# Kernel tuning notes

Measured on AMD Instinct MI355X. Metric: run time of the kernel, lower is better.

## Reference

```python
import jax, jax.numpy as jnp
import numpy as np

B, LQ, S, D, H = 8, 1024, 256, 1024, 16
HD = D // H
LN_EPS = 1e-5


def layer_norm(x, g, b):
    m = jnp.mean(x, axis=-1, keepdims=True)
    v = jnp.mean((x - m) ** 2, axis=-1, keepdims=True)
    return (x - m) / jnp.sqrt(v + LN_EPS) * g + b


def setup_inputs() -> dict:
    key = jax.random.key(0)
    ks = jax.random.split(key, 12)
    sc = 0.02
    p = lambda k, shp: jax.random.normal(k, shp, dtype=jnp.float32) * sc
    return {
        "memory": jax.random.normal(ks[0], (B, LQ, D // 2), dtype=jnp.float32),
        "gaze_features": jax.random.normal(ks[1], (B, LQ, D // 2), dtype=jnp.float32),
        "text_features": jax.random.normal(ks[2], (B, S, D), dtype=jnp.float32),
        "w_in": p(ks[3], (3 * D, D)),  # packed q,k,v in_proj (torch MHA layout)
        "b_in": jnp.zeros((3 * D,), jnp.float32),
        "w_o": p(ks[4], (D, D)),
        "b_o": jnp.zeros((D,), jnp.float32),
        "w1": p(ks[5], (D, D)),
        "b1": jnp.zeros((D,), jnp.float32),
        "w2": p(ks[6], (D, D)),
        "b2": jnp.zeros((D,), jnp.float32),
        "g1": jnp.ones((D,), jnp.float32),
        "be1": jnp.zeros((D,), jnp.float32),
        "g2": jnp.ones((D,), jnp.float32),
        "be2": jnp.zeros((D,), jnp.float32),
    }


def reference(memory, gaze_features, text_features, w_in, b_in, w_o, b_o,
              w1, b1, w2, b2, g1, be1, g2, be2):
    combined = jnp.concatenate([memory, gaze_features], axis=-1)  # [B, LQ, D]
    wq, wk, wv = w_in[:D], w_in[D:2 * D], w_in[2 * D:]
    bq, bk, bv = b_in[:D], b_in[D:2 * D], b_in[2 * D:]

    q = (combined @ wq.T + bq).reshape(B, LQ, H, HD)
    k = (text_features @ wk.T + bk).reshape(B, S, H, HD)
    v = (text_features @ wv.T + bv).reshape(B, S, H, HD)

    scores = jnp.einsum("bqhd,bkhd->bhqk", q, k) / jnp.sqrt(jnp.float32(HD))
    attn_w = jax.nn.softmax(scores, axis=-1)
    ctx = jnp.einsum("bhqk,bkhd->bqhd", attn_w, v).reshape(B, LQ, D)
    attn_output = ctx @ w_o.T + b_o  # [B, LQ, D]

    # dual FFN branches share linear1/linear2 (as in the source); dropout = eval identity
    ffn = jax.nn.relu(attn_output @ w1.T + b1) @ w2.T + b2
    refpoint_embed = layer_norm(ffn, g1, be1)
    tgt = layer_norm(ffn, g2, be2)

    # vectorized box decode (replaces the per-element Python loop)
    s = jax.nn.sigmoid(attn_output[..., :4])
    xc, yc, w, h = s[..., 0], s[..., 1], s[..., 2], s[..., 3]
    init_box_proposal = jnp.stack(
        [xc - w / 2, yc - h / 2, xc + w / 2, yc + h / 2], axis=-1)  # [B, LQ, 4]

    return refpoint_embed, tgt, init_box_proposal
```

## Files before the change

kernel.cpp:

```cpp
#include <hip/hip_runtime.h>


typedef unsigned short u16;
typedef unsigned int u32;
typedef __bf16 bf16x8 __attribute__((ext_vector_type(8)));
typedef float f32x4 __attribute__((ext_vector_type(4)));
typedef u16 u16x4 __attribute__((ext_vector_type(4)));

struct CvtArgs { const void* in[15]; };

__device__ __forceinline__ u16 f2bf(float f) {
  u32 u = __builtin_bit_cast(u32, f);
  u += 0x7fffu + ((u >> 16) & 1u);
  return (u16)(u >> 16);
}
__device__ __forceinline__ float bf2f(u16 h) {
  u32 u = ((u32)h) << 16;
  return __builtin_bit_cast(float, u);
}

struct WsPtrs {
  u16 *c_mem, *c_gaze, *c_text, *c_win, *c_bin, *c_wo, *c_bo, *c_w1, *c_b1,
      *c_w2, *c_b2, *c_g1, *c_be1, *c_g2, *c_be2;
  u16 *q, *k, *v, *ctx, *woT, *wf, *bfb, *h1, *ffnb;
};
__device__ __forceinline__ WsPtrs wsp(u16* C) {
  WsPtrs w;
  w.c_mem = C;                 w.c_gaze = C + 4194304;   w.c_text = C + 8388608;
  w.c_win = C + 10485760;      w.c_bin = C + 13631488;   w.c_wo = C + 13634560;
  w.c_bo = C + 14683136;       w.c_w1 = C + 14684160;    w.c_b1 = C + 15732736;
  w.c_w2 = C + 15733760;       w.c_b2 = C + 16782336;    w.c_g1 = C + 16783360;
  w.c_be1 = C + 16784384;      w.c_g2 = C + 16785408;    w.c_be2 = C + 16786432;
  u16* B2 = C + 16787488;
  w.q = B2;                    w.k = B2 + 8388608;       w.v = B2 + 10485760;
  w.ctx = B2 + 12582912;
  w.woT = B2 + 20971520;
  w.wf  = B2 + 22020096;
  w.bfb = B2 + 23068672;
  w.h1  = B2 + 29360128;
  w.ffnb = B2;
  return w;
}

__device__ __forceinline__ void cvt_chunk(bool f32in, u16* dst,
                                          const void* const* srcs, u32 c8) {
  const u32 cum[16] = {0u, 4194304u, 8388608u, 10485760u, 13631488u, 13634560u,
                       14683136u, 14684160u, 15732736u, 15733760u, 16782336u,
                       16783360u, 16784384u, 16785408u, 16786432u, 16787456u};
  u32 base = c8 * 8u;
  int idx = 0;
#pragma unroll
  for (int i = 1; i < 15; ++i) if (base >= cum[i]) idx = i;
  u32 off = base - cum[idx];
  if (f32in) {
    const float* s = (const float*)srcs[idx] + off;
    float4 a = ((const float4*)s)[0];
    float4 b = ((const float4*)s)[1];
    u16 t[8] = {f2bf(a.x), f2bf(a.y), f2bf(a.z), f2bf(a.w),
                f2bf(b.x), f2bf(b.y), f2bf(b.z), f2bf(b.w)};
    *(uint4*)(dst + base) = *(const uint4*)t;
  } else {
    *(uint4*)(dst + base) = *(const uint4*)((const u16*)srcs[idx] + off);
  }
}

__global__ __launch_bounds__(256) void cvt_tr(CvtArgs a, u16* ws) {
  __shared__ u16 tile[128 * 136];
  const bool f32in = (((const u32*)a.in[11])[0] == 0x3F800000u);
  const int bid = blockIdx.x, tid = threadIdx.x;
  if (bid < 64) {
    WsPtrs w = wsp(ws);
    int tr = bid >> 3, tc = bid & 7;
#pragma unroll
    for (int p = 0; p < 8; ++p) {
      int t = p * 16 + (tid >> 4);
      int j8 = (tid & 15) * 8;
      u16 tmp[8];
      if (f32in) {
        const float* s = (const float*)a.in[5] + (size_t)(tr * 128 + t) * 1024 + tc * 128 + j8;
        float4 x = ((const float4*)s)[0], y = ((const float4*)s)[1];
        tmp[0]=f2bf(x.x); tmp[1]=f2bf(x.y); tmp[2]=f2bf(x.z); tmp[3]=f2bf(x.w);
        tmp[4]=f2bf(y.x); tmp[5]=f2bf(y.y); tmp[6]=f2bf(y.z); tmp[7]=f2bf(y.w);
      } else {
        *(uint4*)tmp = *(const uint4*)((const u16*)a.in[5] + (size_t)(tr * 128 + t) * 1024 + tc * 128 + j8);
      }
      *(uint4*)&tile[t * 136 + j8] = *(const uint4*)tmp;
    }
    __syncthreads();
#pragma unroll
    for (int p = 0; p < 8; ++p) {
      int j = p * 16 + (tid >> 4);
      int t8 = (tid & 15) * 8;
      u16 tmp[8];
#pragma unroll
      for (int i = 0; i < 8; ++i) tmp[i] = tile[(t8 + i) * 136 + j];
      *(uint4*)(w.woT + (size_t)(tc * 128 + j) * 1024 + tr * 128 + t8) = *(const uint4*)tmp;
    }
  } else {
    u32 c8 = (u32)(bid - 64) * 256u + tid;
    if (c8 < 2098432u) cvt_chunk(f32in, ws, a.in, c8);
  }
}

template <int TN>
__device__ __forceinline__ void gemm_core(
    u16* sA, u16* sB,
    const u16* A0, const u16* A1, int Ksplit, int lda0, int lda1,
    const u16* W, const u16* bias, void* out, int N, int K,
    int mode, int lg, int m0, int n0)
{
  constexpr int JN = TN >> 5;
  constexpr int BCPT = TN >> 5;
  const int tid = threadIdx.x;
  const int wave = tid >> 6, lane = tid & 63;
  const int quad = lane >> 4, l16 = lane & 15;
  const int wm = wave >> 1, wn = wave & 1;

  f32x4 acc[4][JN];
#pragma unroll
  for (int i = 0; i < 4; ++i)
#pragma unroll
    for (int j = 0; j < JN; ++j) acc[i][j] = (f32x4){0.f, 0.f, 0.f, 0.f};

  for (int k0 = 0; k0 < K; k0 += 64) {
#pragma unroll
    for (int qi = 0; qi < 4; ++qi) {
      int p = (wave * 4 + qi) * 64 + lane;
      int row = p >> 3;
      int c = (p & 7) ^ (row & 7);
      int gk = k0 + (c << 3);
      const u16* srcA = (gk < Ksplit) ? (A0 + (size_t)(m0 + row) * lda0 + gk)
                                      : (A1 + (size_t)(m0 + row) * lda1 + (gk - Ksplit));
      __builtin_amdgcn_global_load_lds(
          (const __attribute__((address_space(1))) void*)srcA,
          (__attribute__((address_space(3))) void*)&sA[(size_t)(wave * 4 + qi) * 512],
          16, 0, 0);
    }
#pragma unroll
    for (int qi = 0; qi < BCPT; ++qi) {
      int p = (wave * BCPT + qi) * 64 + lane;
      int row = p >> 3;
      int c = (p & 7) ^ (row & 7);
      int gk = k0 + (c << 3);
      const u16* srcB = W + (size_t)(n0 + row) * K + gk;
      __builtin_amdgcn_global_load_lds(
          (const __attribute__((address_space(1))) void*)srcB,
          (__attribute__((address_space(3))) void*)&sB[(size_t)(wave * BCPT + qi) * 512],
          16, 0, 0);
    }
    __syncthreads();
#pragma unroll
    for (int ks = 0; ks < 2; ++ks) {
      const int ch = (ks << 2) + quad;
      bf16x8 af[4], bw[JN];
#pragma unroll
      for (int i = 0; i < 4; ++i) {
        int row = wm * 64 + i * 16 + l16;
        af[i] = *(const bf16x8*)&sA[(row << 6) + ((ch ^ (row & 7)) << 3)];
      }
#pragma unroll
      for (int j = 0; j < JN; ++j) {
        int row = wn * (TN >> 1) + j * 16 + l16;
        bw[j] = *(const bf16x8*)&sB[(row << 6) + ((ch ^ (row & 7)) << 3)];
      }
#pragma unroll
      for (int i = 0; i < 4; ++i)
#pragma unroll
        for (int j = 0; j < JN; ++j)
          acc[i][j] = __builtin_amdgcn_mfma_f32_16x16x32_bf16(af[i], bw[j], acc[i][j], 0, 0, 0);
    }
    __syncthreads();
  }

#pragma unroll
  for (int i = 0; i < 4; ++i) {
#pragma unroll
    for (int j = 0; j < JN; ++j) {
      int n = n0 + wn * (TN >> 1) + j * 16 + l16;
      float bv = bias ? bf2f(bias[n]) : 0.f;
#pragma unroll
      for (int rr = 0; rr < 4; ++rr) {
        int m = m0 + wm * 64 + i * 16 + quad * 4 + rr;
        float val = acc[i][j][rr] + bv;
        if (mode == 1) val = fmaxf(val, 0.f);
        if (mode <= 1) {
          ((u16*)out)[(size_t)m * N + n] = f2bf(val);
        } else if (mode == 3) {
          int b = m >> lg, l = m & ((1 << lg) - 1);
          int h = n >> 6, d = n & 63;
          ((u16*)out)[((size_t)((b * 16 + h)) << (lg + 6)) + (l << 6) + d] = f2bf(val);
        } else {
          int b = m >> lg, s = m & ((1 << lg) - 1);
          int h = n >> 6, d = n & 63;
          ((u16*)out)[((size_t)(((b * 16 + h) << 6) + d) << lg) + s] = f2bf(val);
        }
      }
    }
  }
}

__device__ __forceinline__ int xswz(int u, int n8) {
  return (u & 7) * n8 + (u >> 3);
}

__global__ __launch_bounds__(256, 4) void qkvwf(u16* ws) {
  __shared__ __align__(16) u16 lds[16384];
  WsPtrs w = wsp(ws);
  const int bid = blockIdx.x, tid = threadIdx.x;
  if (bid < 512) {
    int u = xswz(bid, 64);
    gemm_core<128>(lds, lds + 8192, w.c_mem, w.c_gaze, 512, 512, 512,
                   w.c_win, w.c_bin, w.q, 1024, 1024, 3, 10,
                   (u >> 3) * 128, (u & 7) * 128);
  } else if (bid < 640) {
    int u = xswz(bid - 512, 16);
    gemm_core<128>(lds, lds + 8192, w.c_text, w.c_text, 1024, 1024, 1024,
                   w.c_win + 1048576, w.c_bin + 1024, w.k, 1024, 1024, 3, 8,
                   (u >> 3) * 128, (u & 7) * 128);
  } else if (bid < 768) {
    int u = xswz(bid - 640, 16);
    gemm_core<128>(lds, lds + 8192, w.c_text, w.c_text, 1024, 1024, 1024,
                   w.c_win + 2097152, w.c_bin + 2048, w.v, 1024, 1024, 4, 8,
                   (u >> 3) * 128, (u & 7) * 128);
  } else if (bid < 832) {
    int u = xswz(bid - 768, 8);
    gemm_core<128>(lds, lds + 8192, w.c_w1, w.c_w1, 1024, 1024, 1024,
                   w.woT, nullptr, w.wf, 1024, 1024, 0, 0,
                   (u >> 3) * 128, (u & 7) * 128);
  } else {
    int i = (bid - 832) * 256 + tid;
    const u16* w1row = w.c_w1 + (size_t)i * 1024;
    float acc = bf2f(w.c_b1[i]);
    for (int kk = 0; kk < 1024; kk += 8) {
      bf16x8 wv = *(const bf16x8*)(w1row + kk);
      bf16x8 bv = *(const bf16x8*)(w.c_bo + kk);
#pragma unroll
      for (int j = 0; j < 8; ++j) acc += (float)wv[j] * (float)bv[j];
    }
    w.bfb[i] = f2bf(acc);
  }
}

__global__ __launch_bounds__(256) void attn_kernel(u16* ws) {
  __shared__ u16 sV[64 * 256];
  __shared__ u16 sKP[256 * 64];
  WsPtrs w = wsp(ws);
  const int tid = threadIdx.x;
  const int wave = tid >> 6, lane = tid & 63;
  const int quad = lane >> 4, l16 = lane & 15;
  const int su = xswz(blockIdx.x, 256);
  const int qb = su & 15, bh = su >> 4;

  {
    int rr = tid >> 3, c8 = (tid & 7) << 3;
    const u16* kb = w.k + (size_t)bh * 16384;
#pragma unroll
    for (int p = 0; p < 8; ++p) {
      int row = p * 32 + rr;
      uint4 val = *(const uint4*)(kb + row * 64 + c8);
      *(uint4*)&sKP[(row << 6) + ((((c8 >> 3) ^ (row & 7))) << 3)] = val;
    }
    int r2 = tid >> 5, c8b = (tid & 31) << 3;
    const u16* vb = w.v + (size_t)bh * 16384;
#pragma unroll
    for (int p = 0; p < 8; ++p) {
      int row = p * 8 + r2;
      uint4 val = *(const uint4*)(vb + (row << 8) + c8b);
      *(uint4*)&sV[(row << 8) + ((((c8b >> 3) ^ (row & 7))) << 3)] = val;
    }
  }
  bf16x8 aq[2];
  {
    const u16* qrow = w.q + ((size_t)bh * 1024 + qb * 64 + wave * 16 + l16) * 64 + quad * 8;
    aq[0] = *(const bf16x8*)(qrow);
    aq[1] = *(const bf16x8*)(qrow + 32);
  }
  __syncthreads();

  f32x4 sc[16];
#pragma unroll
  for (int nt = 0; nt < 16; ++nt) sc[nt] = (f32x4){0.f, 0.f, 0.f, 0.f};
  __builtin_amdgcn_s_setprio(1);
#pragma unroll
  for (int ks = 0; ks < 2; ++ks) {
    const int ch = (ks << 2) + quad;
#pragma unroll
    for (int nt = 0; nt < 16; ++nt) {
      int row = nt * 16 + l16;
      bf16x8 bk = *(const bf16x8*)&sKP[(row << 6) + ((ch ^ (row & 7)) << 3)];
      sc[nt] = __builtin_amdgcn_mfma_f32_16x16x32_bf16(aq[ks], bk, sc[nt], 0, 0, 0);
    }
  }
  __builtin_amdgcn_s_setprio(0);
#pragma unroll
  for (int rr = 0; rr < 4; ++rr) {
    float mx = -1e30f;
#pragma unroll
    for (int nt = 0; nt < 16; ++nt) mx = fmaxf(mx, sc[nt][rr]);
    for (int off = 1; off < 16; off <<= 1) mx = fmaxf(mx, __shfl_xor(mx, off, 64));
    float sum = 0.f;
#pragma unroll
    for (int nt = 0; nt < 16; ++nt) {
      float p = __expf((sc[nt][rr] - mx) * 0.125f);
      sc[nt][rr] = p; sum += p;
    }
    for (int off = 1; off < 16; off <<= 1) sum += __shfl_xor(sum, off, 64);
    float inv = 1.f / sum;
#pragma unroll
    for (int nt = 0; nt < 16; ++nt) sc[nt][rr] *= inv;
  }
  __syncthreads();
#pragma unroll
  for (int nt = 0; nt < 16; ++nt)
#pragma unroll
    for (int rr = 0; rr < 4; ++rr) {
      int row = wave * 16 + quad * 4 + rr;
      int col = nt * 16 + l16;
      sKP[(row << 8) + (((col >> 3) ^ (row & 7)) << 3) + (col & 7)] = f2bf(sc[nt][rr]);
    }
  __syncthreads();

  f32x4 o[4];
#pragma unroll
  for (int j = 0; j < 4; ++j) o[j] = (f32x4){0.f, 0.f, 0.f, 0.f};
  __builtin_amdgcn_s_setprio(1);
#pragma unroll
  for (int ks = 0; ks < 8; ++ks) {
    const int ch = (ks << 2) + quad;
    int prow = wave * 16 + l16;
    bf16x8 ap = *(const bf16x8*)&sKP[(prow << 8) + ((ch ^ (prow & 7)) << 3)];
#pragma unroll
    for (int j = 0; j < 4; ++j) {
      int vrow = j * 16 + l16;
      bf16x8 bv = *(const bf16x8*)&sV[(vrow << 8) + ((ch ^ (vrow & 7)) << 3)];
      o[j] = __builtin_amdgcn_mfma_f32_16x16x32_bf16(ap, bv, o[j], 0, 0, 0);
    }
  }
  __builtin_amdgcn_s_setprio(0);
  const int b = bh >> 4, h = bh & 15;
#pragma unroll
  for (int j = 0; j < 4; ++j)
#pragma unroll
    for (int rr = 0; rr < 4; ++rr) {
      int m = qb * 64 + wave * 16 + quad * 4 + rr;
      int d = h * 64 + j * 16 + l16;
      w.ctx[((size_t)b * 1024 + m) * 1024 + d] = f2bf(o[j][rr]);
    }
}

__global__ __launch_bounds__(256, 4) void h1box(u16* ws, void* out, const void* g1orig) {
  __shared__ __align__(16) u16 lds[12288];
  WsPtrs w = wsp(ws);
  const int u = blockIdx.x, tid = threadIdx.x;
  {
    const bool f32out = (((const u32*)g1orig)[0] == 0x3F800000u);
    int m = u * 8 + (tid >> 5);
    int l32 = tid & 31;
    int k0 = l32 * 32;
    const u16* crow = w.ctx + (size_t)m * 1024 + k0;
    float a0 = 0.f, a1 = 0.f, a2 = 0.f, a3 = 0.f;
#pragma unroll
    for (int kk = 0; kk < 32; kk += 8) {
      bf16x8 cv = *(const bf16x8*)(crow + kk);
      bf16x8 w0 = *(const bf16x8*)(w.c_wo + k0 + kk);
      bf16x8 w1v = *(const bf16x8*)(w.c_wo + 1024 + k0 + kk);
      bf16x8 w2v = *(const bf16x8*)(w.c_wo + 2048 + k0 + kk);
      bf16x8 w3v = *(const bf16x8*)(w.c_wo + 3072 + k0 + kk);
#pragma unroll
      for (int j = 0; j < 8; ++j) {
        float c = (float)cv[j];
        a0 += c * (float)w0[j]; a1 += c * (float)w1v[j];
        a2 += c * (float)w2v[j]; a3 += c * (float)w3v[j];
      }
    }
    for (int off = 1; off < 32; off <<= 1) {
      a0 += __shfl_xor(a0, off, 64); a1 += __shfl_xor(a1, off, 64);
      a2 += __shfl_xor(a2, off, 64); a3 += __shfl_xor(a3, off, 64);
    }
    if (l32 == 0) {
      a0 += bf2f(w.c_bo[0]); a1 += bf2f(w.c_bo[1]);
      a2 += bf2f(w.c_bo[2]); a3 += bf2f(w.c_bo[3]);
      float s0 = 1.f / (1.f + __expf(-a0)), s1 = 1.f / (1.f + __expf(-a1));
      float s2 = 1.f / (1.f + __expf(-a2)), s3 = 1.f / (1.f + __expf(-a3));
      float o0 = s0 - s2 * 0.5f, o1 = s1 - s3 * 0.5f;
      float o2 = s0 + s2 * 0.5f, o3 = s1 + s3 * 0.5f;
      if (f32out) {
        float* fo = (float*)out + 16777216;
        *(float4*)(fo + (size_t)m * 4) = make_float4(o0, o1, o2, o3);
      } else {
        u16* bo = (u16*)out + 16777216;
        u16x4 o; o[0] = f2bf(o0); o[1] = f2bf(o1); o[2] = f2bf(o2); o[3] = f2bf(o3);
        *(u16x4*)(bo + (size_t)m * 4) = o;
      }
    }
  }
  int us = xswz(u, 128);
  gemm_core<64>(lds, lds + 8192, w.ctx, w.ctx, 1024, 1024, 1024,
                w.wf, w.bfb, w.h1, 1024, 1024, 1, 0,
                (us >> 4) * 128, (us & 15) * 64);
}

__global__ __launch_bounds__(256, 4) void w2gemm(u16* ws) {
  __shared__ __align__(16) u16 lds[12288];
  WsPtrs w = wsp(ws);
  int us = xswz((int)blockIdx.x, 128);
  gemm_core<64>(lds, lds + 8192, w.h1, w.h1, 1024, 1024, 1024,
                w.c_w2, w.c_b2, w.ffnb, 1024, 1024, 0, 0,
                (us >> 4) * 128, (us & 15) * 64);
}

__global__ __launch_bounds__(256) void ln_kernel(u16* ws, void* outv, const void* g1orig) {
  WsPtrs w = wsp(ws);
  const bool f32out = (((const u32*)g1orig)[0] == 0x3F800000u);
  const int row = blockIdx.x, tid = threadIdx.x;
  int c = tid * 4;
  u16x4 xr = *(const u16x4*)(w.ffnb + (size_t)row * 1024 + c);
  float x[4] = {bf2f(xr[0]), bf2f(xr[1]), bf2f(xr[2]), bf2f(xr[3])};
  float s = x[0] + x[1] + x[2] + x[3];
  float s2 = x[0]*x[0] + x[1]*x[1] + x[2]*x[2] + x[3]*x[3];
  for (int m = 32; m >= 1; m >>= 1) { s += __shfl_xor(s, m, 64); s2 += __shfl_xor(s2, m, 64); }
  __shared__ float red[8];
  int wv = tid >> 6;
  if ((tid & 63) == 0) { red[wv] = s; red[4 + wv] = s2; }
  __syncthreads();
  s = red[0] + red[1] + red[2] + red[3];
  s2 = red[4] + red[5] + red[6] + red[7];
  float mean = s * (1.f / 1024.f);
  float var = s2 * (1.f / 1024.f) - mean * mean;
  float inv = rsqrtf(var + 1e-5f);
  float y[4] = {(x[0] - mean) * inv, (x[1] - mean) * inv, (x[2] - mean) * inv, (x[3] - mean) * inv};
  float v1[4], v2[4];
#pragma unroll
  for (int i = 0; i < 4; ++i) {
    v1[i] = y[i] * bf2f(w.c_g1[c + i]) + bf2f(w.c_be1[c + i]);
    v2[i] = y[i] * bf2f(w.c_g2[c + i]) + bf2f(w.c_be2[c + i]);
  }
  if (f32out) {
    float* fo = (float*)outv;
    *(float4*)(fo + (size_t)row * 1024 + c) = make_float4(v1[0], v1[1], v1[2], v1[3]);
    *(float4*)(fo + 8388608 + (size_t)row * 1024 + c) = make_float4(v2[0], v2[1], v2[2], v2[3]);
  } else {
    u16* out = (u16*)outv;
    u16x4 o1, o2;
#pragma unroll
    for (int i = 0; i < 4; ++i) { o1[i] = f2bf(v1[i]); o2[i] = f2bf(v2[i]); }
    *(u16x4*)(out + (size_t)row * 1024 + c) = o1;
    *(u16x4*)(out + 8388608 + (size_t)row * 1024 + c) = o2;
  }
}

extern "C" void kernel_launch(void* const* d_in, const int* in_sizes, int n_in,
                              void* d_out, int out_size, void* d_ws, size_t ws_size,
                              hipStream_t stream) {
  CvtArgs ca;
  for (int i = 0; i < 15; ++i) ca.in[i] = d_in[i];
  u16* ws = (u16*)d_ws;
  dim3 blk(256);
  cvt_tr<<<dim3(8261), blk, 0, stream>>>(ca, ws);
  qkvwf<<<dim3(836), blk, 0, stream>>>(ws);
  attn_kernel<<<dim3(2048), blk, 0, stream>>>(ws);
  h1box<<<dim3(1024), blk, 0, stream>>>(ws, d_out, d_in[11]);
  w2gemm<<<dim3(1024), blk, 0, stream>>>(ws);
  ln_kernel<<<dim3(8192), blk, 0, stream>>>(ws, d_out, d_in[11]);
}
```

Baseline: 290.4 us.

## Shrink QKV GEMM tiles to 64x128 and batch conversion chunks per thread

The shared GEMM core is re-parameterised by M tile (TM with TN = 192 - TM), so the QKV/weight-fold GEMMs now use 64x128 tiles with twice as many blocks, less LDS and a higher occupancy bound. The later GEMMs keep their 128x64 tiles through the new template. The conversion kernel now handles four chunks per thread, which cuts its grid by about four times. The aim is better CU fill and less launch/block overhead, at the cost of lower per-block data reuse in the QKV GEMMs.

After: 324.2 us. 11.7% more time.

```diff
diff --git a/kernel.cpp b/kernel.cpp
--- a/kernel.cpp
+++ b/kernel.cpp
@@ -97,35 +97,43 @@
       *(uint4*)(w.woT + (size_t)(tc * 128 + j) * 1024 + tr * 128 + t8) = *(const uint4*)tmp;
     }
   } else {
-    u32 c8 = (u32)(bid - 64) * 256u + tid;
-    if (c8 < 2098432u) cvt_chunk(f32in, ws, a.in, c8);
-  }
-}
-
-template <int TN>
+    u32 b = (u32)(bid - 64) * 1024u + tid;
+#pragma unroll
+    for (int k = 0; k < 4; ++k) {
+      u32 c8 = b + (u32)k * 256u;
+      if (c8 < 2098432u) cvt_chunk(f32in, ws, a.in, c8);
+    }
+  }
+}
+
+template <int TM>
 __device__ __forceinline__ void gemm_core(
-    u16* sA, u16* sB,
+    u16* lds,
     const u16* A0, const u16* A1, int Ksplit, int lda0, int lda1,
     const u16* W, const u16* bias, void* out, int N, int K,
     int mode, int lg, int m0, int n0)
 {
-  constexpr int JN = TN >> 5;
+  constexpr int TN = 192 - TM;
+  constexpr int ACPT = TM >> 5;
   constexpr int BCPT = TN >> 5;
+  u16* sA = lds;
+  u16* sB = lds + TM * 64;
   const int tid = threadIdx.x;
   const int wave = tid >> 6, lane = tid & 63;
   const int quad = lane >> 4, l16 = lane & 15;
-  const int wm = wave >> 1, wn = wave & 1;
-
-  f32x4 acc[4][JN];
+  const int wm = (TM == 128) ? (wave >> 1) : 0;
+  const int wn = (TM == 128) ? (wave & 1) : wave;
+
+  f32x4 acc[4][2];
 #pragma unroll
   for (int i = 0; i < 4; ++i)
 #pragma unroll
-    for (int j = 0; j < JN; ++j) acc[i][j] = (f32x4){0.f, 0.f, 0.f, 0.f};
+    for (int j = 0; j < 2; ++j) acc[i][j] = (f32x4){0.f, 0.f, 0.f, 0.f};
 
   for (int k0 = 0; k0 < K; k0 += 64) {
 #pragma unroll
-    for (int qi = 0; qi < 4; ++qi) {
-      int p = (wave * 4 + qi) * 64 + lane;
+    for (int qi = 0; qi < ACPT; ++qi) {
+      int p = (wave * ACPT + qi) * 64 + lane;
       int row = p >> 3;
       int c = (p & 7) ^ (row & 7);
       int gk = k0 + (c << 3);
@@ -133,7 +141,7 @@
                                       : (A1 + (size_t)(m0 + row) * lda1 + (gk - Ksplit));
       __builtin_amdgcn_global_load_lds(
           (const __attribute__((address_space(1))) void*)srcA,
-          (__attribute__((address_space(3))) void*)&sA[(size_t)(wave * 4 + qi) * 512],
+          (__attribute__((address_space(3))) void*)&sA[(size_t)(wave * ACPT + qi) * 512],
           16, 0, 0);
     }
 #pragma unroll
@@ -152,21 +160,21 @@
 #pragma unroll
     for (int ks = 0; ks < 2; ++ks) {
       const int ch = (ks << 2) + quad;
-      bf16x8 af[4], bw[JN];
+      bf16x8 af[4], bw[2];
 #pragma unroll
       for (int i = 0; i < 4; ++i) {
         int row = wm * 64 + i * 16 + l16;
         af[i] = *(const bf16x8*)&sA[(row << 6) + ((ch ^ (row & 7)) << 3)];
       }
 #pragma unroll
-      for (int j = 0; j < JN; ++j) {
-        int row = wn * (TN >> 1) + j * 16 + l16;
+      for (int j = 0; j < 2; ++j) {
+        int row = wn * 32 + j * 16 + l16;
         bw[j] = *(const bf16x8*)&sB[(row << 6) + ((ch ^ (row & 7)) << 3)];
       }
 #pragma unroll
       for (int i = 0; i < 4; ++i)
 #pragma unroll
-        for (int j = 0; j < JN; ++j)
+        for (int j = 0; j < 2; ++j)
           acc[i][j] = __builtin_amdgcn_mfma_f32_16x16x32_bf16(af[i], bw[j], acc[i][j], 0, 0, 0);
     }
     __syncthreads();
@@ -175,8 +183,8 @@
 #pragma unroll
   for (int i = 0; i < 4; ++i) {
 #pragma unroll
-    for (int j = 0; j < JN; ++j) {
-      int n = n0 + wn * (TN >> 1) + j * 16 + l16;
+    for (int j = 0; j < 2; ++j) {
+      int n = n0 + wn * 32 + j * 16 + l16;
       float bv = bias ? bf2f(bias[n]) : 0.f;
 #pragma unroll
       for (int rr = 0; rr < 4; ++rr) {
@@ -203,32 +211,32 @@
   return (u & 7) * n8 + (u >> 3);
 }
 
-__global__ __launch_bounds__(256, 4) void qkvwf(u16* ws) {
-  __shared__ __align__(16) u16 lds[16384];
+__global__ __launch_bounds__(256, 6) void qkvwf(u16* ws) {
+  __shared__ __align__(16) u16 lds[12288];
   WsPtrs w = wsp(ws);
   const int bid = blockIdx.x, tid = threadIdx.x;
-  if (bid < 512) {
-    int u = xswz(bid, 64);
-    gemm_core<128>(lds, lds + 8192, w.c_mem, w.c_gaze, 512, 512, 512,
-                   w.c_win, w.c_bin, w.q, 1024, 1024, 3, 10,
-                   (u >> 3) * 128, (u & 7) * 128);
-  } else if (bid < 640) {
-    int u = xswz(bid - 512, 16);
-    gemm_core<128>(lds, lds + 8192, w.c_text, w.c_text, 1024, 1024, 1024,
-                   w.c_win + 1048576, w.c_bin + 1024, w.k, 1024, 1024, 3, 8,
-                   (u >> 3) * 128, (u & 7) * 128);
-  } else if (bid < 768) {
-    int u = xswz(bid - 640, 16);
-    gemm_core<128>(lds, lds + 8192, w.c_text, w.c_text, 1024, 1024, 1024,
-                   w.c_win + 2097152, w.c_bin + 2048, w.v, 1024, 1024, 4, 8,
-                   (u >> 3) * 128, (u & 7) * 128);
-  } else if (bid < 832) {
-    int u = xswz(bid - 768, 8);
-    gemm_core<128>(lds, lds + 8192, w.c_w1, w.c_w1, 1024, 1024, 1024,
-                   w.woT, nullptr, w.wf, 1024, 1024, 0, 0,
-                   (u >> 3) * 128, (u & 7) * 128);
+  if (bid < 1024) {
+    int u = xswz(bid, 128);
+    gemm_core<64>(lds, w.c_mem, w.c_gaze, 512, 512, 512,
+                  w.c_win, w.c_bin, w.q, 1024, 1024, 3, 10,
+                  (u >> 3) * 64, (u & 7) * 128);
+  } else if (bid < 1280) {
+    int u = xswz(bid - 1024, 32);
+    gemm_core<64>(lds, w.c_text, w.c_text, 1024, 1024, 1024,
+                  w.c_win + 1048576, w.c_bin + 1024, w.k, 1024, 1024, 3, 8,
+                  (u >> 3) * 64, (u & 7) * 128);
+  } else if (bid < 1536) {
+    int u = xswz(bid - 1280, 32);
+    gemm_core<64>(lds, w.c_text, w.c_text, 1024, 1024, 1024,
+                  w.c_win + 2097152, w.c_bin + 2048, w.v, 1024, 1024, 4, 8,
+                  (u >> 3) * 64, (u & 7) * 128);
+  } else if (bid < 1664) {
+    int u = xswz(bid - 1536, 16);
+    gemm_core<64>(lds, w.c_w1, w.c_w1, 1024, 1024, 1024,
+                  w.woT, nullptr, w.wf, 1024, 1024, 0, 0,
+                  (u >> 3) * 64, (u & 7) * 128);
   } else {
-    int i = (bid - 832) * 256 + tid;
+    int i = (bid - 1664) * 256 + tid;
     const u16* w1row = w.c_w1 + (size_t)i * 1024;
     float acc = bf2f(w.c_b1[i]);
     for (int kk = 0; kk < 1024; kk += 8) {
@@ -395,18 +403,18 @@
     }
   }
   int us = xswz(u, 128);
-  gemm_core<64>(lds, lds + 8192, w.ctx, w.ctx, 1024, 1024, 1024,
-                w.wf, w.bfb, w.h1, 1024, 1024, 1, 0,
-                (us >> 4) * 128, (us & 15) * 64);
+  gemm_core<128>(lds, w.ctx, w.ctx, 1024, 1024, 1024,
+                 w.wf, w.bfb, w.h1, 1024, 1024, 1, 0,
+                 (us >> 4) * 128, (us & 15) * 64);
 }
 
 __global__ __launch_bounds__(256, 4) void w2gemm(u16* ws) {
   __shared__ __align__(16) u16 lds[12288];
   WsPtrs w = wsp(ws);
   int us = xswz((int)blockIdx.x, 128);
-  gemm_core<64>(lds, lds + 8192, w.h1, w.h1, 1024, 1024, 1024,
-                w.c_w2, w.c_b2, w.ffnb, 1024, 1024, 0, 0,
-                (us >> 4) * 128, (us & 15) * 64);
+  gemm_core<128>(lds, w.h1, w.h1, 1024, 1024, 1024,
+                 w.c_w2, w.c_b2, w.ffnb, 1024, 1024, 0, 0,
+                 (us >> 4) * 128, (us & 15) * 64);
 }
 
 __global__ __launch_bounds__(256) void ln_kernel(u16* ws, void* outv, const void* g1orig) {
@@ -456,8 +464,8 @@
   for (int i = 0; i < 15; ++i) ca.in[i] = d_in[i];
   u16* ws = (u16*)d_ws;
   dim3 blk(256);
-  cvt_tr<<<dim3(8261), blk, 0, stream>>>(ca, ws);
-  qkvwf<<<dim3(836), blk, 0, stream>>>(ws);
+  cvt_tr<<<dim3(2114), blk, 0, stream>>>(ca, ws);
+  qkvwf<<<dim3(1668), blk, 0, stream>>>(ws);
   attn_kernel<<<dim3(2048), blk, 0, stream>>>(ws);
   h1box<<<dim3(1024), blk, 0, stream>>>(ws, d_out, d_in[11]);
   w2gemm<<<dim3(1024), blk, 0, stream>>>(ws);
```
